# Kernel tuning notes

Hardware: AMD Instinct MI355X
Metric: run time of the kernel (lower is better)

## Reference

```python
import jax, jax.numpy as jnp
import numpy as np
import math

NUM_CLUSTERS = 3


def _maxpool_last(x, k=9, pad=4):
    # torch MaxPool with default stride=kernel_size; pad positions are -inf
    nd = x.ndim
    return jax.lax.reduce_window(
        x, -jnp.inf, jax.lax.max,
        (1,) * (nd - 1) + (k,),
        (1,) * (nd - 1) + (k,),
        [(0, 0)] * (nd - 1) + [(pad, pad)],
    )


def setup_inputs() -> dict:
    key = jax.random.key(0)
    ks = jax.random.split(key, 8)
    b, h, l, dk = 36, 8, 1152, 72
    dm = h * dk  # 576 == d_model
    c = NUM_CLUSTERS
    f = lambda k_, sh: jax.random.normal(k_, sh, jnp.float32)
    return {
        "Q": f(ks[0], (b, h, l, dk)),
        "K": f(ks[1], (b, h, l, dk)),
        "V": f(ks[2], (b, h, l, dk)),
        "Wp": f(ks[3], (dm, c)) * 0.05, "bp": jnp.zeros((c,), jnp.float32),
        "Wck": f(ks[4], (c, c)) * 0.5, "bck": jnp.zeros((c,), jnp.float32),
        "Wcq": f(ks[5], (c, c)) * 0.5, "bcq": jnp.zeros((c,), jnp.float32),
        "Wb": f(ks[6], (c, dm)) * 0.05, "bb": jnp.zeros((dm,), jnp.float32),
    }


def reference(Q, K, V, Wp, bp, Wck, bck, Wcq, bcq, Wb, bb):
    b, h, l, dk = Q.shape
    dm = h * dk
    c = NUM_CLUSTERS
    b2 = b // 2

    # MaxPool1d(kernel=9, stride=9, pad=4) applied to raw reshape (b, dk*h, l)
    Kp = _maxpool_last(K.reshape(b, dm, l)).reshape(b, h, -1, dk)
    Vp = _maxpool_last(V.reshape(b, dm, l)).reshape(b, h, -1, dk)
    l_k = Kp.shape[2]

    # pad batch dim with zeros, then unfold dim0 with window b/2, step 1
    K_padded = jnp.concatenate(
        [jnp.zeros((b2, h, l_k, dk), Q.dtype), Kp[1:]], axis=0)  # (b2+b-1, h, l_k, dk)
    idx = jnp.arange(b)[:, None] + jnp.arange(b2)[None, :]  # (b, b2)
    # torch unfold puts window dim last: (b, h, l_k, dk, b2)
    K_unf = jnp.transpose(K_padded[idx], (0, 2, 3, 4, 1)).reshape(b, l_k, b2, dm)

    cluster_k_p = jax.nn.relu(K_unf @ Wp + bp)          # (b, l_k, b2, c)
    cluster_k = jax.nn.softmax(cluster_k_p @ Wck + bck, axis=-1)
    cluster_q = jax.nn.softmax(cluster_k_p @ Wcq + bcq, axis=-1)

    mu = jnp.mean(cluster_q, axis=-1)                    # (b, l_k, b2)
    sigma = jax.nn.softplus(jnp.std(cluster_q, axis=-1, ddof=1))  # torch std unbiased
    xk = jnp.mean(cluster_k, axis=-1)
    log_prob = (-0.5 * jnp.square((xk - mu) / sigma)
                - jnp.log(sigma) - 0.5 * math.log(2.0 * math.pi))
    # CrossEntropyLoss(mu, mu): soft targets over class dim 1 (l_k), mean over rest
    ce = jnp.mean(-jnp.sum(mu * jax.nn.log_softmax(mu, axis=1), axis=1))
    loss = -jnp.mean(log_prob) + ce

    scores = jnp.einsum('blpc,bluc->blpu', cluster_q, cluster_k) / c  # (b,l_k,b2,b2)
    mask = jnp.triu(jnp.ones((b2, b2), bool), k=1)
    scores = jnp.where(mask, jnp.float32(-1e9), scores)
    attn = jax.nn.softmax(scores, axis=-1)
    cluster_q2 = jnp.einsum('blpu,bluc->blpc', attn, cluster_q)       # (b,l_k,b2,c)

    cluster_center = jax.nn.relu(cluster_q2 @ Wb + bb)                # (b,l_k,b2,dm)
    # MaxPool2d(kernel=(1,9), stride=(1,9), pad=(0,4)) over last dim
    cluster_center = _maxpool_last(cluster_center)                    # (b,l_k,b2,ceil(dm/9))
    cluster_center = cluster_center.reshape(b, h, -1, l_k, dk)        # raw reshape

    scores_center = jnp.einsum('bhqd,bhckd->bhqk', Q, cluster_center)  # (b,h,l,l_k)
    attn2 = jax.nn.softmax(scores_center, axis=-1)
    context = jnp.einsum('bhqk,bhkd->bhqd', attn2, Vp)
    return context, loss
```

## Files before the change

kernel.cpp:

```cpp
#include <hip/hip_runtime.h>
#include <math.h>

#define BATCH 36
#define H 8
#define L 1152
#define DK 72
#define DM 576
#define LK 128
#define B2 18
#define NC 3

#define POOL_PER_B (DM*LK)
#define POOL_TOTAL (BATCH*POOL_PER_B)
#define CLUS_TOTAL (BATCH*LK*B2)
#define CCPOOL_PER_B (LK*B2*64)
#define CTX_ELEMS (BATCH*H*L*DK)
#define NBH (BATCH*H)

typedef __attribute__((ext_vector_type(8))) short short8;
typedef __attribute__((ext_vector_type(4))) float f32x4;

__device__ __forceinline__ unsigned short bf16_rne(float x) {
  unsigned u = __float_as_uint(x);
  unsigned r = u + 0x7FFFu + ((u >> 16) & 1u);
  return (unsigned short)(r >> 16);
}
__device__ __forceinline__ unsigned pack2(float a, float b) {
  return (unsigned)bf16_rne(a) | ((unsigned)bf16_rne(b) << 16);
}
__device__ __forceinline__ float max9(float x0, float x1, float x2, float x3,
                                      float x4, float x5, float x6, float x7,
                                      float x8) {
  float m0 = fmaxf(fmaxf(x0, x1), x2);
  float m1 = fmaxf(fmaxf(x3, x4), x5);
  float m2 = fmaxf(fmaxf(x6, x7), x8);
  return fmaxf(fmaxf(m0, m1), m2);
}

__global__ __launch_bounds__(256, 8) void pool_kernel(
    const float* __restrict__ Kin, const float* __restrict__ Vin,
    float* __restrict__ pK, float* __restrict__ pV) {
  int t = blockIdx.x * 256 + threadIdx.x;
  const int perT = (BATCH * DM) * 32;
  const float* src;
  float* dst;
  if (t < perT) {
    src = Kin; dst = pK;
  } else {
    src = Vin; dst = pV; t -= perT;
  }
  int row = t >> 5, g = t & 31;
  const float* p = src + (size_t)row * L + g * 36;

  float4 a[9];
#pragma unroll
  for (int k = 0; k < 8; ++k) a[k + 1] = *(const float4*)(p + k * 4);
  a[0] = (g > 0) ? *(const float4*)(p - 4)
                 : make_float4(-INFINITY, -INFINITY, -INFINITY, -INFINITY);
  __builtin_amdgcn_sched_barrier(0);

  float w0 = max9(a[0].x, a[0].y, a[0].z, a[0].w,
                  a[1].x, a[1].y, a[1].z, a[1].w, a[2].x);
  float w1 = max9(a[2].y, a[2].z, a[2].w,
                  a[3].x, a[3].y, a[3].z, a[3].w, a[4].x, a[4].y);
  float w2 = max9(a[4].z, a[4].w,
                  a[5].x, a[5].y, a[5].z, a[5].w, a[6].x, a[6].y, a[6].z);
  float w3 = max9(a[6].w,
                  a[7].x, a[7].y, a[7].z, a[7].w,
                  a[8].x, a[8].y, a[8].z, a[8].w);

  *(float4*)(dst + (size_t)row * LK + g * 4) = make_float4(w0, w1, w2, w3);
}

__global__ __launch_bounds__(256) void cluster_kernel(
    const float* __restrict__ pK,
    const float* __restrict__ Wp,  const float* __restrict__ bp,
    const float* __restrict__ Wck, const float* __restrict__ bck,
    const float* __restrict__ Wcq, const float* __restrict__ bcq,
    float* __restrict__ cq_out, float* __restrict__ ck_out,
    float* __restrict__ loss_acc) {
  int bb = blockIdx.x / 9;
  int s  = blockIdx.x % 9;
  int tid = threadIdx.x;

  __shared__ float sK[256 * 33];
  __shared__ float sWp[1728];
  __shared__ float red[256];

  for (int i = tid; i < 1728; i += 256) sWp[i] = Wp[i];

  float a0 = 0.f, a1 = 0.f, a2 = 0.f;
  int umin = (bb >= 18) ? 0 : (18 - bb);

  for (int u = umin; u < 18; ++u) {
    int b2 = bb + u - 17;
    __syncthreads();
    const float4* src = (const float4*)(pK + (size_t)b2 * POOL_PER_B + s * 8192);
#pragma unroll
    for (int k = 0; k < 8; ++k) {
      int i = tid + k * 256;
      float4 v = src[i];
      int base = i * 4;
      float* dst = &sK[(base >> 5) * 33 + (base & 31)];
      dst[0] = v.x; dst[1] = v.y; dst[2] = v.z; dst[3] = v.w;
    }
    __syncthreads();
    const float* wrow = &sWp[u * 3];
    const float* krow = &sK[tid * 33];
#pragma unroll
    for (int g = 0; g < 32; ++g) {
      float v = krow[g];
      a0 = fmaf(v, wrow[g * 54 + 0], a0);
      a1 = fmaf(v, wrow[g * 54 + 1], a1);
      a2 = fmaf(v, wrow[g * 54 + 2], a2);
    }
  }

  float p0 = fmaxf(a0 + bp[0], 0.f);
  float p1 = fmaxf(a1 + bp[1], 0.f);
  float p2 = fmaxf(a2 + bp[2], 0.f);

  float k0 = p0 * Wck[0] + p1 * Wck[3] + p2 * Wck[6] + bck[0];
  float k1 = p0 * Wck[1] + p1 * Wck[4] + p2 * Wck[7] + bck[1];
  float k2 = p0 * Wck[2] + p1 * Wck[5] + p2 * Wck[8] + bck[2];
  float mk = fmaxf(k0, fmaxf(k1, k2));
  float e0 = __expf(k0 - mk), e1 = __expf(k1 - mk), e2 = __expf(k2 - mk);
  float inv = 1.f / (e0 + e1 + e2);
  float ck0 = e0 * inv, ck1 = e1 * inv, ck2 = e2 * inv;

  float q0 = p0 * Wcq[0] + p1 * Wcq[3] + p2 * Wcq[6] + bcq[0];
  float q1 = p0 * Wcq[1] + p1 * Wcq[4] + p2 * Wcq[7] + bcq[1];
  float q2 = p0 * Wcq[2] + p1 * Wcq[5] + p2 * Wcq[8] + bcq[2];
  float mq = fmaxf(q0, fmaxf(q1, q2));
  float f0 = __expf(q0 - mq), f1 = __expf(q1 - mq), f2 = __expf(q2 - mq);
  float invq = 1.f / (f0 + f1 + f2);
  float cq0 = f0 * invq, cq1 = f1 * invq, cq2 = f2 * invq;

  size_t t = (size_t)bb * 2304 + s * 256 + tid;
  ck_out[t * 3 + 0] = ck0;
  ck_out[t * 3 + 1] = ck1;
  ck_out[t * 3 + 2] = ck2;
  cq_out[t * 3 + 0] = cq0;
  cq_out[t * 3 + 1] = cq1;
  cq_out[t * 3 + 2] = cq2;

  float mean = (cq0 + cq1 + cq2) * (1.f / 3.f);
  float d0 = cq0 - mean, d1 = cq1 - mean, d2 = cq2 - mean;
  float var = (d0 * d0 + d1 * d1 + d2 * d2) * 0.5f;
  float sd  = sqrtf(var);
  float sig = log1pf(__expf(sd));
  float ls  = logf(sig);

  __syncthreads();
  red[tid] = ls;
  __syncthreads();
  for (int r = 128; r > 0; r >>= 1) {
    if (tid < r) red[tid] += red[tid + r];
    __syncthreads();
  }
  if (tid == 0) atomicAdd(loss_acc, red[0]);
}

__global__ __launch_bounds__(256) void center_kernel(
    const float* __restrict__ cq, const float* __restrict__ ck,
    const float* __restrict__ Wb, const float* __restrict__ bbias,
    float* __restrict__ ccpool) {
  int blk = blockIdx.x;
  int bb  = blk / LK;
  int lk2 = blk % LK;
  int tid = threadIdx.x;

  __shared__ float scq[54], sck[54], sq2[54];
  __shared__ float sWb[3 * 576];
  __shared__ float sbb[576];

  const float* cqb = cq + ((size_t)bb * (LK * B2) + (size_t)lk2 * B2) * 3;
  const float* ckb = ck + ((size_t)bb * (LK * B2) + (size_t)lk2 * B2) * 3;
  if (tid < 54) { scq[tid] = cqb[tid]; sck[tid] = ckb[tid]; }
  for (int i = tid; i < 1728; i += 256) sWb[i] = Wb[i];
  for (int i = tid; i < 576; i += 256) sbb[i] = bbias[i];
  __syncthreads();

  if (tid < B2) {
    int p = tid;
    float s[B2];
    float g0 = scq[p * 3 + 0], g1 = scq[p * 3 + 1], g2 = scq[p * 3 + 2];
    float mx = -INFINITY;
#pragma unroll
    for (int u = 0; u < B2; ++u) {
      float sv = (g0 * sck[u * 3] + g1 * sck[u * 3 + 1] + g2 * sck[u * 3 + 2]) *
                 (1.f / 3.f);
      if (u > p) sv = -1e9f;
      s[u] = sv;
      mx = fmaxf(mx, sv);
    }
    float sum = 0.f;
#pragma unroll
    for (int u = 0; u < B2; ++u) { s[u] = __expf(s[u] - mx); sum += s[u]; }
    float inv = 1.f / sum;
    float o0 = 0.f, o1 = 0.f, o2 = 0.f;
#pragma unroll
    for (int u = 0; u < B2; ++u) {
      float a = s[u] * inv;
      o0 = fmaf(a, scq[u * 3 + 0], o0);
      o1 = fmaf(a, scq[u * 3 + 1], o1);
      o2 = fmaf(a, scq[u * 3 + 2], o2);
    }
    sq2[p * 3 + 0] = o0; sq2[p * 3 + 1] = o1; sq2[p * 3 + 2] = o2;
  }
  __syncthreads();

  float* outb = ccpool + (size_t)bb * CCPOOL_PER_B + (size_t)lk2 * (B2 * 64);
  for (int i = tid; i < B2 * 64; i += 256) {
    int p = i >> 6;
    int w = i & 63;
    float g0 = sq2[p * 3 + 0], g1 = sq2[p * 3 + 1], g2 = sq2[p * 3 + 2];
    int t0 = w * 9 - 4;
    int lo = t0 < 0 ? 0 : t0;
    int hi = t0 + 8; if (hi > 575) hi = 575;
    float mxv = -INFINITY;
    for (int tt = lo; tt <= hi; ++tt) {
      float cv = g0 * sWb[tt] + g1 * sWb[576 + tt] + g2 * sWb[1152 + tt] + sbb[tt];
      cv = fmaxf(cv, 0.f);
      mxv = fmaxf(mxv, cv);
    }
    outb[i] = mxv;
  }
}

#define CFRAG_T (NBH*8*3*64)
#define VFRAG_T (NBH*5*4*64)
__global__ __launch_bounds__(256) void prep_kernel(
    const float* __restrict__ ccpool, const float* __restrict__ pV,
    uint4* __restrict__ Cfrag, uint4* __restrict__ Vfrag) {
  int t = blockIdx.x * 256 + threadIdx.x;
  unsigned short hi[8];
  if (t < CFRAG_T) {
    int lane = t & 63;
    int rest = t >> 6;
    int ks = rest % 3;
    int mtb = rest / 3;
    int mt = mtb & 7;
    int bh = mtb >> 3;
    int bb = bh >> 3, hh = bh & 7;
    int key = mt * 16 + (lane & 15);
    int d0 = ks * 32 + (lane >> 4) * 8;
    const float* cp = ccpool + (size_t)bb * CCPOOL_PER_B + hh * 18432 + key * 72;
#pragma unroll
    for (int j = 0; j < 8; ++j) {
      int d = d0 + j;
      float v = (d < 72) ? (cp[d] + cp[9216 + d]) : 0.f;
      hi[j] = bf16_rne(v);
    }
    uint4 h4;
    h4.x = hi[0] | (hi[1] << 16); h4.y = hi[2] | (hi[3] << 16);
    h4.z = hi[4] | (hi[5] << 16); h4.w = hi[6] | (hi[7] << 16);
    Cfrag[t] = h4;
  } else {
    int t2 = t - CFRAG_T;
    int lane = t2 & 63;
    int rest = t2 >> 6;
    int ks = rest & 3;
    int ntb = rest >> 2;
    int nt = ntb % 5;
    int bh = ntb / 5;
    int d = nt * 16 + (lane & 15);
    int k0 = ks * 32 + (lane >> 4) * 8;
    const float* vp = pV + (size_t)bh * (LK * DK);
#pragma unroll
    for (int j = 0; j < 8; ++j) {
      int k = k0 + j;
      float v = (d < 72) ? vp[k * 72 + d] : 0.f;
      hi[j] = bf16_rne(v);
    }
    uint4 h4;
    h4.x = hi[0] | (hi[1] << 16); h4.y = hi[2] | (hi[3] << 16);
    h4.z = hi[4] | (hi[5] << 16); h4.w = hi[6] | (hi[7] << 16);
    Vfrag[t2] = h4;
  }
}

__global__ __launch_bounds__(256) void attn2_kernel(
    const float* __restrict__ Q, const uint4* __restrict__ Cfrag,
    const uint4* __restrict__ Vfrag, float* __restrict__ out) {
  __shared__ __align__(16) uint4 sFrag[2816];

  int bh = blockIdx.x / 9, qt = blockIdx.x % 9;
  int tid = threadIdx.x;
  int wid = tid >> 6, lane = tid & 63;
  int lq = lane & 15, lg = lane >> 4;
  int qbase = qt * 128 + wid * 32;

  const uint4* gC = Cfrag + (size_t)bh * 1536;
  const uint4* gV = Vfrag + (size_t)bh * 1280;
#pragma unroll
  for (int k = 0; k < 6; ++k) sFrag[tid + k * 256] = gC[tid + k * 256];
#pragma unroll
  for (int k = 0; k < 5; ++k) sFrag[1536 + tid + k * 256] = gV[tid + k * 256];
  __syncthreads();

  f32x4 sacc[2][8];
#pragma unroll
  for (int s = 0; s < 2; ++s)
#pragma unroll
    for (int mt = 0; mt < 8; ++mt) sacc[s][mt] = (f32x4){0.f, 0.f, 0.f, 0.f};

#pragma unroll
  for (int ks = 0; ks < 3; ++ks) {
    short8 qh[2];
#pragma unroll
    for (int s = 0; s < 2; ++s) {
      int q = qbase + s * 16 + lq;
      const float* qrow = Q + ((size_t)bh * L + q) * DK;
      int d0 = ks * 32 + lg * 8;
      float x[8];
      if (ks < 2) {
        float4 a = *(const float4*)(qrow + d0);
        float4 b = *(const float4*)(qrow + d0 + 4);
        x[0] = a.x; x[1] = a.y; x[2] = a.z; x[3] = a.w;
        x[4] = b.x; x[5] = b.y; x[6] = b.z; x[7] = b.w;
      } else {
        if (lg == 0) {
          float4 a = *(const float4*)(qrow + 64);
          float4 b = *(const float4*)(qrow + 68);
          x[0] = a.x; x[1] = a.y; x[2] = a.z; x[3] = a.w;
          x[4] = b.x; x[5] = b.y; x[6] = b.z; x[7] = b.w;
        } else {
#pragma unroll
          for (int j = 0; j < 8; ++j) x[j] = 0.f;
        }
      }
#pragma unroll
      for (int j = 0; j < 8; ++j) qh[s][j] = (short)bf16_rne(x[j]);
    }
#pragma unroll
    for (int mt = 0; mt < 8; ++mt) {
      short8 chi = *(const short8*)&sFrag[(mt * 3 + ks) * 64 + lane];
#pragma unroll
      for (int s = 0; s < 2; ++s)
        sacc[s][mt] = __builtin_amdgcn_mfma_f32_16x16x32_bf16(chi, qh[s], sacc[s][mt], 0, 0, 0);
    }
  }

  unsigned pw[2][8][2];
#pragma unroll
  for (int s = 0; s < 2; ++s) {
    float mx = -INFINITY;
#pragma unroll
    for (int mt = 0; mt < 8; ++mt)
#pragma unroll
      for (int r = 0; r < 4; ++r) mx = fmaxf(mx, sacc[s][mt][r]);
    mx = fmaxf(mx, __shfl_xor(mx, 16));
    mx = fmaxf(mx, __shfl_xor(mx, 32));
    float sum = 0.f;
#pragma unroll
    for (int mt = 0; mt < 8; ++mt)
#pragma unroll
      for (int r = 0; r < 4; ++r) {
        float p = __expf(sacc[s][mt][r] - mx);
        sacc[s][mt][r] = p;
        sum += p;
      }
    sum += __shfl_xor(sum, 16);
    sum += __shfl_xor(sum, 32);
    float inv = 1.f / sum;
#pragma unroll
    for (int mt = 0; mt < 8; ++mt) {
      pw[s][mt][0] = pack2(sacc[s][mt][0] * inv, sacc[s][mt][1] * inv);
      pw[s][mt][1] = pack2(sacc[s][mt][2] * inv, sacc[s][mt][3] * inv);
    }
  }

  f32x4 oacc[2][5];
#pragma unroll
  for (int s = 0; s < 2; ++s)
#pragma unroll
    for (int nt = 0; nt < 5; ++nt) oacc[s][nt] = (f32x4){0.f, 0.f, 0.f, 0.f};

  int baseA = lq + 32 * (lg & 1);
  int baseB = baseA + 16;
  bool hiGrp = (lg & 2) != 0;

#pragma unroll
  for (int ks = 0; ks < 4; ++ks) {
    short8 pa[2];
#pragma unroll
    for (int s = 0; s < 2; ++s) {
      unsigned a0 = pw[s][2 * ks][0],     a1 = pw[s][2 * ks][1];
      unsigned b0 = pw[s][2 * ks + 1][0], b1 = pw[s][2 * ks + 1][1];
      unsigned r00 = __shfl(a0, baseA, 64), r10 = __shfl(b0, baseA, 64);
      unsigned r01 = __shfl(a1, baseA, 64), r11 = __shfl(b1, baseA, 64);
      unsigned r02 = __shfl(a0, baseB, 64), r12 = __shfl(b0, baseB, 64);
      unsigned r03 = __shfl(a1, baseB, 64), r13 = __shfl(b1, baseB, 64);
      uint4 u;
      u.x = hiGrp ? r10 : r00;
      u.y = hiGrp ? r11 : r01;
      u.z = hiGrp ? r12 : r02;
      u.w = hiGrp ? r13 : r03;
      pa[s] = *(short8*)&u;
    }
#pragma unroll
    for (int nt = 0; nt < 5; ++nt) {
      short8 vhi = *(const short8*)&sFrag[1536 + (nt * 4 + ks) * 64 + lane];
#pragma unroll
      for (int s = 0; s < 2; ++s)
        oacc[s][nt] = __builtin_amdgcn_mfma_f32_16x16x32_bf16(pa[s], vhi, oacc[s][nt], 0, 0, 0);
    }
  }

#pragma unroll
  for (int s = 0; s < 2; ++s) {
#pragma unroll
    for (int nt = 0; nt < 5; ++nt) {
      int d = nt * 16 + lq;
      if (d < 72) {
        float* orow = out + ((size_t)bh * L + qbase + s * 16 + lg * 4) * DK + d;
#pragma unroll
        for (int r = 0; r < 4; ++r) orow[(size_t)r * DK] = oacc[s][nt][r];
      }
    }
  }
}

__global__ void finalize_kernel(const float* __restrict__ loss_acc,
                                float* __restrict__ out_loss) {
  *out_loss = loss_acc[0] * (1.f / 82944.f) + 207.93889646f;
}

extern "C" void kernel_launch(void* const* d_in, const int* in_sizes, int n_in,
                              void* d_out, int out_size, void* d_ws, size_t ws_size,
                              hipStream_t stream) {
  const float* Q    = (const float*)d_in[0];
  const float* Kin  = (const float*)d_in[1];
  const float* Vin  = (const float*)d_in[2];
  const float* Wp   = (const float*)d_in[3];
  const float* bp   = (const float*)d_in[4];
  const float* Wck  = (const float*)d_in[5];
  const float* bck  = (const float*)d_in[6];
  const float* Wcq  = (const float*)d_in[7];
  const float* bcq  = (const float*)d_in[8];
  const float* Wb   = (const float*)d_in[9];
  const float* bbv  = (const float*)d_in[10];
  float* out = (float*)d_out;

  float* ws = (float*)d_ws;
  float* pK       = ws;
  float* pV       = pK + POOL_TOTAL;
  float* cq       = pV + POOL_TOTAL;
  float* ck       = cq + (size_t)CLUS_TOTAL * 3;
  float* ccpool   = ck + (size_t)CLUS_TOTAL * 3;
  float* cfrag_f  = ccpool + (size_t)BATCH * CCPOOL_PER_B;
  uint4* Cfrag    = (uint4*)cfrag_f;
  uint4* Vfrag    = Cfrag + (size_t)CFRAG_T;
  float* loss_acc = (float*)(Vfrag + (size_t)VFRAG_T);

  hipMemsetAsync(loss_acc, 0, sizeof(float), stream);

  pool_kernel<<<2 * (BATCH * DM) * 32 / 256, 256, 0, stream>>>(Kin, Vin, pK, pV);
  cluster_kernel<<<BATCH * 9, 256, 0, stream>>>(
      pK, Wp, bp, Wck, bck, Wcq, bcq, cq, ck, loss_acc);
  center_kernel<<<BATCH * LK, 256, 0, stream>>>(cq, ck, Wb, bbv, ccpool);
  prep_kernel<<<(CFRAG_T + VFRAG_T) / 256, 256, 0, stream>>>(ccpool, pV, Cfrag, Vfrag);
  attn2_kernel<<<NBH * 9, 256, 0, stream>>>(Q, Cfrag, Vfrag, out);
  finalize_kernel<<<1, 1, 0, stream>>>(loss_acc, out + CTX_ELEMS);
}
```

Before: 195.4 us.

## Fuse cluster-center pooling with bf16 fragment packing and fold loss finalize into prep

The center kernel now processes the two lk rows that sum into each key tile (per batch, head and key tile). It keeps pooled values in shared memory and writes bf16 MFMA fragments for C directly, which removes the fp32 ccpool round trip through global memory and the C half of the prep kernel. The loss finalize is folded into the V-prep kernel to remove one launch. The fused kernel issues fewer blocks, and its final packing stage uses only 192 of 256 threads.

```diff
diff --git a/kernel.cpp b/kernel.cpp
--- a/kernel.cpp
+++ b/kernel.cpp
@@ -13,7 +13,6 @@
 #define POOL_PER_B (DM*LK)
 #define POOL_TOTAL (BATCH*POOL_PER_B)
 #define CLUS_TOTAL (BATCH*LK*B2)
-#define CCPOOL_PER_B (LK*B2*64)
 #define CTX_ELEMS (BATCH*H*L*DK)
 #define NBH (BATCH*H)
 
@@ -161,60 +160,68 @@
   if (tid == 0) atomicAdd(loss_acc, red[0]);
 }
 
-__global__ __launch_bounds__(256) void center_kernel(
+__global__ __launch_bounds__(256) void center2_kernel(
     const float* __restrict__ cq, const float* __restrict__ ck,
     const float* __restrict__ Wb, const float* __restrict__ bbias,
-    float* __restrict__ ccpool) {
-  int blk = blockIdx.x;
-  int bb  = blk / LK;
-  int lk2 = blk % LK;
+    uint4* __restrict__ Cfrag) {
+  int bid = blockIdx.x;
+  int mt = bid & 7, hh = (bid >> 3) & 7, bb = bid >> 6;
+  int L0 = hh * 16 + mt;
   int tid = threadIdx.x;
 
-  __shared__ float scq[54], sck[54], sq2[54];
-  __shared__ float sWb[3 * 576];
+  __shared__ float sWb[1728];
   __shared__ float sbb[576];
-
-  const float* cqb = cq + ((size_t)bb * (LK * B2) + (size_t)lk2 * B2) * 3;
-  const float* ckb = ck + ((size_t)bb * (LK * B2) + (size_t)lk2 * B2) * 3;
-  if (tid < 54) { scq[tid] = cqb[tid]; sck[tid] = ckb[tid]; }
+  __shared__ float scq[2][54], sck[2][54], sq2[2][54];
+  __shared__ float pooled[2][1152];
+
   for (int i = tid; i < 1728; i += 256) sWb[i] = Wb[i];
   for (int i = tid; i < 576; i += 256) sbb[i] = bbias[i];
-  __syncthreads();
-
-  if (tid < B2) {
-    int p = tid;
-    float s[B2];
-    float g0 = scq[p * 3 + 0], g1 = scq[p * 3 + 1], g2 = scq[p * 3 + 2];
-    float mx = -INFINITY;
-#pragma unroll
-    for (int u = 0; u < B2; ++u) {
-      float sv = (g0 * sck[u * 3] + g1 * sck[u * 3 + 1] + g2 * sck[u * 3 + 2]) *
-                 (1.f / 3.f);
-      if (u > p) sv = -1e9f;
-      s[u] = sv;
-      mx = fmaxf(mx, sv);
-    }
-    float sum = 0.f;
-#pragma unroll
-    for (int u = 0; u < B2; ++u) { s[u] = __expf(s[u] - mx); sum += s[u]; }
-    float inv = 1.f / sum;
-    float o0 = 0.f, o1 = 0.f, o2 = 0.f;
-#pragma unroll
-    for (int u = 0; u < B2; ++u) {
-      float a = s[u] * inv;
-      o0 = fmaf(a, scq[u * 3 + 0], o0);
-      o1 = fmaf(a, scq[u * 3 + 1], o1);
-      o2 = fmaf(a, scq[u * 3 + 2], o2);
-    }
-    sq2[p * 3 + 0] = o0; sq2[p * 3 + 1] = o1; sq2[p * 3 + 2] = o2;
-  }
-  __syncthreads();
-
-  float* outb = ccpool + (size_t)bb * CCPOOL_PER_B + (size_t)lk2 * (B2 * 64);
-  for (int i = tid; i < B2 * 64; i += 256) {
-    int p = i >> 6;
-    int w = i & 63;
-    float g0 = sq2[p * 3 + 0], g1 = sq2[p * 3 + 1], g2 = sq2[p * 3 + 2];
+  if (tid < 108) {
+    int h2 = tid / 54, r = tid % 54;
+    int Lx = L0 + h2 * 8;
+    const float* cqb = cq + ((size_t)bb * 2304 + Lx * 18) * 3;
+    const float* ckb = ck + ((size_t)bb * 2304 + Lx * 18) * 3;
+    scq[h2][r] = cqb[r];
+    sck[h2][r] = ckb[r];
+  }
+  __syncthreads();
+
+  {
+    int h2 = tid >> 6;
+    int p  = tid & 63;
+    if (h2 < 2 && p < B2) {
+      float s[B2];
+      float g0 = scq[h2][p * 3 + 0], g1 = scq[h2][p * 3 + 1], g2 = scq[h2][p * 3 + 2];
+      float mx = -INFINITY;
+#pragma unroll
+      for (int u = 0; u < B2; ++u) {
+        float sv = (g0 * sck[h2][u * 3] + g1 * sck[h2][u * 3 + 1] +
+                    g2 * sck[h2][u * 3 + 2]) * (1.f / 3.f);
+        if (u > p) sv = -1e9f;
+        s[u] = sv;
+        mx = fmaxf(mx, sv);
+      }
+      float sum = 0.f;
+#pragma unroll
+      for (int u = 0; u < B2; ++u) { s[u] = __expf(s[u] - mx); sum += s[u]; }
+      float inv = 1.f / sum;
+      float o0 = 0.f, o1 = 0.f, o2 = 0.f;
+#pragma unroll
+      for (int u = 0; u < B2; ++u) {
+        float a = s[u] * inv;
+        o0 = fmaf(a, scq[h2][u * 3 + 0], o0);
+        o1 = fmaf(a, scq[h2][u * 3 + 1], o1);
+        o2 = fmaf(a, scq[h2][u * 3 + 2], o2);
+      }
+      sq2[h2][p * 3 + 0] = o0; sq2[h2][p * 3 + 1] = o1; sq2[h2][p * 3 + 2] = o2;
+    }
+  }
+  __syncthreads();
+
+  for (int i = tid; i < 2 * 1152; i += 256) {
+    int h2 = i / 1152, r = i % 1152;
+    int p = r >> 6, w = r & 63;
+    float g0 = sq2[h2][p * 3 + 0], g1 = sq2[h2][p * 3 + 1], g2 = sq2[h2][p * 3 + 2];
     int t0 = w * 9 - 4;
     int lo = t0 < 0 ? 0 : t0;
     int hi = t0 + 8; if (hi > 575) hi = 575;
@@ -224,60 +231,61 @@
       cv = fmaxf(cv, 0.f);
       mxv = fmaxf(mxv, cv);
     }
-    outb[i] = mxv;
+    pooled[h2][r] = mxv;
+  }
+  __syncthreads();
+
+  if (tid < 192) {
+    int ks = tid >> 6, lane = tid & 63;
+    int kk = lane & 15;
+    int d0 = ks * 32 + ((lane >> 4) << 3);
+    unsigned short hi8[8];
+#pragma unroll
+    for (int j = 0; j < 8; ++j) {
+      int d = d0 + j;
+      float v = 0.f;
+      if (d < 72) {
+        int idx = kk * 72 + d;
+        v = pooled[0][idx] + pooled[1][idx];
+      }
+      hi8[j] = bf16_rne(v);
+    }
+    uint4 h4;
+    h4.x = hi8[0] | (hi8[1] << 16); h4.y = hi8[2] | (hi8[3] << 16);
+    h4.z = hi8[4] | (hi8[5] << 16); h4.w = hi8[6] | (hi8[7] << 16);
+    int bh = bb * 8 + hh;
+    Cfrag[(((size_t)bh * 8 + mt) * 3 + ks) * 64 + lane] = h4;
   }
 }
 
 #define CFRAG_T (NBH*8*3*64)
 #define VFRAG_T (NBH*5*4*64)
-__global__ __launch_bounds__(256) void prep_kernel(
-    const float* __restrict__ ccpool, const float* __restrict__ pV,
-    uint4* __restrict__ Cfrag, uint4* __restrict__ Vfrag) {
-  int t = blockIdx.x * 256 + threadIdx.x;
-  unsigned short hi[8];
-  if (t < CFRAG_T) {
-    int lane = t & 63;
-    int rest = t >> 6;
-    int ks = rest % 3;
-    int mtb = rest / 3;
-    int mt = mtb & 7;
-    int bh = mtb >> 3;
-    int bb = bh >> 3, hh = bh & 7;
-    int key = mt * 16 + (lane & 15);
-    int d0 = ks * 32 + (lane >> 4) * 8;
-    const float* cp = ccpool + (size_t)bb * CCPOOL_PER_B + hh * 18432 + key * 72;
-#pragma unroll
-    for (int j = 0; j < 8; ++j) {
-      int d = d0 + j;
-      float v = (d < 72) ? (cp[d] + cp[9216 + d]) : 0.f;
-      hi[j] = bf16_rne(v);
-    }
-    uint4 h4;
-    h4.x = hi[0] | (hi[1] << 16); h4.y = hi[2] | (hi[3] << 16);
-    h4.z = hi[4] | (hi[5] << 16); h4.w = hi[6] | (hi[7] << 16);
-    Cfrag[t] = h4;
-  } else {
-    int t2 = t - CFRAG_T;
-    int lane = t2 & 63;
-    int rest = t2 >> 6;
-    int ks = rest & 3;
-    int ntb = rest >> 2;
-    int nt = ntb % 5;
-    int bh = ntb / 5;
-    int d = nt * 16 + (lane & 15);
-    int k0 = ks * 32 + (lane >> 4) * 8;
-    const float* vp = pV + (size_t)bh * (LK * DK);
-#pragma unroll
-    for (int j = 0; j < 8; ++j) {
-      int k = k0 + j;
-      float v = (d < 72) ? vp[k * 72 + d] : 0.f;
-      hi[j] = bf16_rne(v);
-    }
-    uint4 h4;
-    h4.x = hi[0] | (hi[1] << 16); h4.y = hi[2] | (hi[3] << 16);
-    h4.z = hi[4] | (hi[5] << 16); h4.w = hi[6] | (hi[7] << 16);
-    Vfrag[t2] = h4;
-  }
+__global__ __launch_bounds__(256) void prep_v_kernel(
+    const float* __restrict__ pV, uint4* __restrict__ Vfrag,
+    const float* __restrict__ loss_acc, float* __restrict__ out_loss) {
+  int t2 = blockIdx.x * 256 + threadIdx.x;
+  if (t2 == 0)
+    *out_loss = loss_acc[0] * (1.f / 82944.f) + 207.93889646f;
+  int lane = t2 & 63;
+  int rest = t2 >> 6;
+  int ks = rest & 3;
+  int ntb = rest >> 2;
+  int nt = ntb % 5;
+  int bh = ntb / 5;
+  int d = nt * 16 + (lane & 15);
+  int k0 = ks * 32 + (lane >> 4) * 8;
+  const float* vp = pV + (size_t)bh * (LK * DK);
+  unsigned short hi8[8];
+#pragma unroll
+  for (int j = 0; j < 8; ++j) {
+    int k = k0 + j;
+    float v = (d < 72) ? vp[k * 72 + d] : 0.f;
+    hi8[j] = bf16_rne(v);
+  }
+  uint4 h4;
+  h4.x = hi8[0] | (hi8[1] << 16); h4.y = hi8[2] | (hi8[3] << 16);
+  h4.z = hi8[4] | (hi8[5] << 16); h4.w = hi8[6] | (hi8[7] << 16);
+  Vfrag[t2] = h4;
 }
 
 __global__ __launch_bounds__(256) void attn2_kernel(
@@ -422,11 +430,6 @@
   }
 }
 
-__global__ void finalize_kernel(const float* __restrict__ loss_acc,
-                                float* __restrict__ out_loss) {
-  *out_loss = loss_acc[0] * (1.f / 82944.f) + 207.93889646f;
-}
-
 extern "C" void kernel_launch(void* const* d_in, const int* in_sizes, int n_in,
                               void* d_out, int out_size, void* d_ws, size_t ws_size,
                               hipStream_t stream) {
@@ -448,9 +451,7 @@
   float* pV       = pK + POOL_TOTAL;
   float* cq       = pV + POOL_TOTAL;
   float* ck       = cq + (size_t)CLUS_TOTAL * 3;
-  float* ccpool   = ck + (size_t)CLUS_TOTAL * 3;
-  float* cfrag_f  = ccpool + (size_t)BATCH * CCPOOL_PER_B;
-  uint4* Cfrag    = (uint4*)cfrag_f;
+  uint4* Cfrag    = (uint4*)(ck + (size_t)CLUS_TOTAL * 3);
   uint4* Vfrag    = Cfrag + (size_t)CFRAG_T;
   float* loss_acc = (float*)(Vfrag + (size_t)VFRAG_T);
 
@@ -459,8 +460,8 @@
   pool_kernel<<<2 * (BATCH * DM) * 32 / 256, 256, 0, stream>>>(Kin, Vin, pK, pV);
   cluster_kernel<<<BATCH * 9, 256, 0, stream>>>(
       pK, Wp, bp, Wck, bck, Wcq, bcq, cq, ck, loss_acc);
-  center_kernel<<<BATCH * LK, 256, 0, stream>>>(cq, ck, Wb, bbv, ccpool);
-  prep_kernel<<<(CFRAG_T + VFRAG_T) / 256, 256, 0, stream>>>(ccpool, pV, Cfrag, Vfrag);
+  center2_kernel<<<BATCH * 64, 256, 0, stream>>>(cq, ck, Wb, bbv, Cfrag);
+  prep_v_kernel<<<VFRAG_T / 256, 256, 0, stream>>>(
+      pV, Vfrag, loss_acc, out + CTX_ELEMS);
   attn2_kernel<<<NBH * 9, 256, 0, stream>>>(Q, Cfrag, Vfrag, out);
-  finalize_kernel<<<1, 1, 0, stream>>>(loss_acc, out + CTX_ELEMS);
-}
+}
```

Result: faster. 184.0 us (-5.8%).
